# Performance work log

Hardware: AMD Instinct MI355X
Metric: run time of the kernel (lower is better)

Reference implementation:

```python
import jax, jax.numpy as jnp
import numpy as np

N_DATA = 131072
N_HID = 32768
D = 256
E1 = 524288  # data -> hidden
E2 = 524288  # hidden -> hidden
E3 = 524288  # hidden -> data


def setup_inputs() -> dict:
    key = jax.random.key(0)
    ks = jax.random.split(key, 32)
    rn = lambda k, shape, s=0.05: (jax.random.normal(k, shape, jnp.float32) * s)
    inp = {
        "data_x": jax.random.normal(ks[0], (N_DATA, 8), jnp.float32),
        "hidden_x": jax.random.normal(ks[1], (N_HID, 3), jnp.float32),
        "dh_src": jax.random.randint(ks[2], (E1,), 0, N_DATA, jnp.int32),
        "dh_dst": jax.random.randint(ks[3], (E1,), 0, N_HID, jnp.int32),
        "hh_src": jax.random.randint(ks[4], (E2,), 0, N_HID, jnp.int32),
        "hh_dst": jax.random.randint(ks[5], (E2,), 0, N_HID, jnp.int32),
        "hd_src": jax.random.randint(ks[6], (E3,), 0, N_HID, jnp.int32),
        "hd_dst": jax.random.randint(ks[7], (E3,), 0, N_DATA, jnp.int32),
        # encoder params
        "enc_src_w": rn(ks[8], (D, 8)), "enc_src_b": rn(ks[9], (D,)),
        "enc_dst_w": rn(ks[10], (D, 3)), "enc_dst_b": rn(ks[11], (D,)),
        "enc_wl": rn(ks[12], (D, D)), "enc_bl": rn(ks[13], (D,)), "enc_wr": rn(ks[14], (D, D)),
        # processor params
        "proc_wl": rn(ks[15], (D, D)), "proc_bl": rn(ks[16], (D,)), "proc_wr": rn(ks[17], (D, D)),
        "proc_mlp_w": rn(ks[18], (D, D)), "proc_mlp_b": rn(ks[19], (D,)),
        # decoder params
        "dec_src_w": rn(ks[20], (D, D)), "dec_src_b": rn(ks[21], (D,)),
        "dec_dst_w": rn(ks[22], (D, 8)), "dec_dst_b": rn(ks[23], (D,)),
        "dec_wl": rn(ks[24], (D, D)), "dec_bl": rn(ks[25], (D,)), "dec_wr": rn(ks[26], (D, D)),
        "out_w": rn(ks[27], (8, D)), "out_b": rn(ks[28], (8,)),
    }
    return inp


def _gelu(x):
    return jax.nn.gelu(x, approximate=False)  # torch nn.GELU default (erf)


def _sage(x_src, x_dst, src, dst, wl, bl, wr, n_dst):
    """PyG SAGEConv, mean aggregation: lin_l(mean_j x_src[j]) + lin_r(x_dst)."""
    msg = x_src[src]                                              # [E, D] gather
    agg = jax.ops.segment_sum(msg, dst, num_segments=n_dst)       # [n_dst, D]
    cnt = jax.ops.segment_sum(jnp.ones((src.shape[0], 1), msg.dtype), dst,
                              num_segments=n_dst)
    mean = agg / jnp.maximum(cnt, 1.0)
    return mean @ wl.T + bl + x_dst @ wr.T


def reference(data_x, hidden_x, dh_src, dh_dst, hh_src, hh_dst, hd_src, hd_dst,
              enc_src_w, enc_src_b, enc_dst_w, enc_dst_b, enc_wl, enc_bl, enc_wr,
              proc_wl, proc_bl, proc_wr, proc_mlp_w, proc_mlp_b,
              dec_src_w, dec_src_b, dec_dst_w, dec_dst_b, dec_wl, dec_bl, dec_wr,
              out_w, out_b):
    # ---- encoder: data -> hidden ----
    h_data = _gelu(data_x @ enc_src_w.T + enc_src_b)
    h_hid = _gelu(hidden_x @ enc_dst_w.T + enc_dst_b)
    h_hid = _gelu(_sage(h_data, h_hid, dh_src, dh_dst, enc_wl, enc_bl, enc_wr, N_HID))
    # ---- processor: hidden -> hidden, then GELU-Linear-GELU MLP ----
    h_hid = _sage(h_hid, h_hid, hh_src, hh_dst, proc_wl, proc_bl, proc_wr, N_HID)
    h_hid = _gelu(_gelu(h_hid) @ proc_mlp_w.T + proc_mlp_b)
    # ---- decoder: hidden -> data ----
    s = _gelu(h_hid @ dec_src_w.T + dec_src_b)
    d = _gelu(data_x @ dec_dst_w.T + dec_dst_b)
    d = _gelu(_sage(s, d, hd_src, hd_dst, dec_wl, dec_bl, dec_wr, N_DATA))
    return d @ out_w.T + out_b  # [N_DATA, 8]
```

## Files before the change

kernel.cpp:

```cpp
#include <hip/hip_runtime.h>
#include <stdint.h>

#define NDATA 131072
#define NHID  32768
#define NEDGE 524288

typedef __bf16 bf16_t;
typedef __bf16 bf16x4 __attribute__((ext_vector_type(4)));
typedef __bf16 bf16x8 __attribute__((ext_vector_type(8)));
typedef float  f32x4  __attribute__((ext_vector_type(4)));

__device__ __forceinline__ float gelu_f(float x) {
    return 0.5f * x * (1.0f + erff(x * 0.7071067811865476f));
}

__device__ __forceinline__ void glds16(const void* g, void* l) {
    auto* gp = reinterpret_cast<const __attribute__((address_space(1))) uint32_t*>(
        reinterpret_cast<uintptr_t>(g));
    auto* lp = reinterpret_cast<__attribute__((address_space(3))) uint32_t*>(
        reinterpret_cast<uintptr_t>(l));
    __builtin_amdgcn_global_load_lds(gp, lp, 16, 0, 0);
}

struct WPtrs { const float* p[9]; };

__global__ __launch_bounds__(256)
void cvt_w_kernel(WPtrs wp, bf16_t* __restrict__ out) {
    const int i = blockIdx.x * 256 + threadIdx.x;
    if (i < 8 * 65536) {
        const int wsel = i >> 16, off = i & 65535;
        out[i] = (bf16_t)wp.p[wsel][off];
    } else {
        out[i] = (bf16_t)wp.p[8][i - 8 * 65536];
    }
}

struct EdgePtrs { const int* src[3]; const int* dst[3]; };

__device__ __forceinline__ int cnt_off_of(int g) { return g == 0 ? 0 : (g == 1 ? NHID : 2 * NHID); }
__device__ __forceinline__ int rp_off_of(int g)  { return g == 0 ? 0 : (g == 1 ? NHID + 1 : 2 * NHID + 2); }
__device__ __forceinline__ int shift_of(int g)   { return g == 2 ? 10 : 8; }

__global__ __launch_bounds__(256)
void hist3(EdgePtrs ep, int* __restrict__ cnt_all) {
    const int g = blockIdx.x >> 11;
    const int i = ((blockIdx.x & 2047) << 8) + threadIdx.x;
    atomicAdd(&cnt_all[cnt_off_of(g) + ep.dst[g][i]], 1);
}

__global__ __launch_bounds__(256)
void scan_blk3(const int* __restrict__ cnt_all, int* __restrict__ pre_all,
               int* __restrict__ blk) {
    __shared__ int sh[256];
    const int bid = blockIdx.x;
    int g, local;
    if (bid < 32)      { g = 0; local = bid; }
    else if (bid < 64) { g = 1; local = bid - 32; }
    else               { g = 2; local = bid - 64; }
    const int t = threadIdx.x;
    const int cbase = cnt_off_of(g) + local * 1024 + t * 4;
    const int pbase = rp_off_of(g)  + local * 1024 + t * 4;
    int4 v = *(const int4*)(cnt_all + cbase);
    sh[t] = v.x + v.y + v.z + v.w;
    __syncthreads();
    for (int off = 1; off < 256; off <<= 1) {
        int other = 0;
        if (t >= off) other = sh[t - off];
        __syncthreads();
        if (t >= off) sh[t] += other;
        __syncthreads();
    }
    const int excl = (t == 0) ? 0 : sh[t - 1];
    int4 o;
    o.x = excl; o.y = o.x + v.x; o.z = o.y + v.y; o.w = o.z + v.z;
    *(int4*)(pre_all + pbase) = o;
    if (t == 255) blk[bid] = sh[255];
}

__global__ __launch_bounds__(256)
void scan_add3(const int* __restrict__ pre_all, const int* __restrict__ blk,
               int* __restrict__ rp_all, int* __restrict__ binA) {
    __shared__ int sh[256];
    const int bid = blockIdx.x;
    int g, local, gbase;
    if (bid < 32)      { g = 0; local = bid;      gbase = 0; }
    else if (bid < 64) { g = 1; local = bid - 32; gbase = 32; }
    else               { g = 2; local = bid - 64; gbase = 64; }
    const int t = threadIdx.x;
    int part = 0;
    if (t < local) part = blk[gbase + t];
    sh[t] = part;
    __syncthreads();
    for (int o2 = 128; o2 > 0; o2 >>= 1) {
        if (t < o2) sh[t] += sh[t + o2];
        __syncthreads();
    }
    const int off = sh[0];
    const int idx = local * 1024 + t * 4;
    const int pbase = rp_off_of(g) + idx;
    int4 v = *(const int4*)(pre_all + pbase);
    v.x += off; v.y += off; v.z += off; v.w += off;
    *(int4*)(rp_all + pbase) = v;
    const int bw = 1 << shift_of(g);
    if ((idx & (bw - 1)) == 0) binA[g * 128 + (idx >> shift_of(g))] = v.x;
    if (local == 0 && t == 0) {
        const int n = (g == 2) ? NDATA : NHID;
        rp_all[rp_off_of(g) + n] = NEDGE;
    }
}

__global__ __launch_bounds__(256)
void partition3(EdgePtrs ep, int* __restrict__ binA, int2* __restrict__ pairs) {
    __shared__ int hist[128], base[128], cur[128];
    const int g = blockIdx.x >> 7;
    const int blk = blockIdx.x & 127;
    const int t = threadIdx.x;
    const int shift = shift_of(g);
    const int e_base = blk * 4096;
    const int* src = ep.src[g];
    const int* dst = ep.dst[g];
    if (t < 128) { hist[t] = 0; cur[t] = 0; }
    __syncthreads();
    #pragma unroll
    for (int it = 0; it < 16; ++it) {
        const int d = dst[e_base + it * 256 + t];
        atomicAdd(&hist[d >> shift], 1);
    }
    __syncthreads();
    if (t < 128) base[t] = atomicAdd(&binA[g * 128 + t], hist[t]);
    __syncthreads();
    #pragma unroll
    for (int it = 0; it < 16; ++it) {
        const int e = e_base + it * 256 + t;
        const int s = src[e], d = dst[e];
        const int b = d >> shift;
        const int l = atomicAdd(&cur[b], 1);
        pairs[(size_t)g * NEDGE + base[b] + l] = make_int2(s, d);
    }
}

__global__ __launch_bounds__(256)
void binsort3(const int2* __restrict__ pairs, const int* __restrict__ rp_all,
              int* __restrict__ sorted_all) {
    __shared__ int cur[1024];
    const int g = blockIdx.x >> 7;
    const int b = blockIdx.x & 127;
    const int t = threadIdx.x;
    const int shift = shift_of(g);
    const int W = 1 << shift;
    const int d0 = b << shift;
    const int rpo = rp_off_of(g);
    for (int i = t; i < W; i += 256) cur[i] = rp_all[rpo + d0 + i];
    __syncthreads();
    const int e0 = rp_all[rpo + d0];
    const int e1 = rp_all[rpo + d0 + W];
    for (int e = e0 + t; e < e1; e += 256) {
        const int2 p = pairs[(size_t)g * NEDGE + e];
        const int pos = atomicAdd(&cur[p.y - d0], 1);
        sorted_all[(size_t)g * NEDGE + pos] = p.x;
    }
}

__global__ __launch_bounds__(256)
void csr_gather_mean(const bf16_t* __restrict__ feat, const int* __restrict__ row_ptr,
                     const int* __restrict__ sorted_src, bf16_t* __restrict__ mean, int n) {
    const int lane = threadIdx.x & 63;
    const int half = lane >> 5;
    const int col8 = (lane & 31) * 8;
    const int w = blockIdx.x * 4 + (threadIdx.x >> 6);
    if (w >= n) return;
    const int e0 = row_ptr[w], e1 = row_ptr[w + 1];
    float acc[8] = {0.f, 0.f, 0.f, 0.f, 0.f, 0.f, 0.f, 0.f};
    int e = e0 + half;
    for (; e + 6 < e1; e += 8) {
        const int s0 = sorted_src[e],     s1 = sorted_src[e + 2];
        const int s2 = sorted_src[e + 4], s3 = sorted_src[e + 6];
        const bf16x8 v0 = *(const bf16x8*)(feat + (size_t)s0 * 256 + col8);
        const bf16x8 v1 = *(const bf16x8*)(feat + (size_t)s1 * 256 + col8);
        const bf16x8 v2 = *(const bf16x8*)(feat + (size_t)s2 * 256 + col8);
        const bf16x8 v3 = *(const bf16x8*)(feat + (size_t)s3 * 256 + col8);
        #pragma unroll
        for (int j = 0; j < 8; ++j)
            acc[j] += ((float)v0[j] + (float)v1[j]) + ((float)v2[j] + (float)v3[j]);
    }
    for (; e < e1; e += 2) {
        const int s0 = sorted_src[e];
        const bf16x8 v0 = *(const bf16x8*)(feat + (size_t)s0 * 256 + col8);
        #pragma unroll
        for (int j = 0; j < 8; ++j) acc[j] += (float)v0[j];
    }
    #pragma unroll
    for (int j = 0; j < 8; ++j) acc[j] += __shfl_xor(acc[j], 32, 64);
    if (half == 0) {
        const float ic = 1.0f / fmaxf((float)(e1 - e0), 1.0f);
        bf16x8 r;
        #pragma unroll
        for (int j = 0; j < 8; ++j) r[j] = (bf16_t)(acc[j] * ic);
        *(bf16x8*)(mean + (size_t)w * 256 + col8) = r;
    }
}

__global__ __launch_bounds__(256)
void enc_both(const float* __restrict__ hx, const float* __restrict__ w3,
              const float* __restrict__ b3, bf16_t* __restrict__ out3,
              const float* __restrict__ dx, const float* __restrict__ w8,
              const float* __restrict__ b8, bf16_t* __restrict__ out8) {
    __shared__ float ws[8 * 256];
    __shared__ float bs[256];
    const int t = threadIdx.x;
    const bool is8 = (blockIdx.x >= 512);
    if (is8) {
        #pragma unroll
        for (int j = 0; j < 8; ++j) ws[j * 256 + t] = w8[t * 8 + j];
        bs[t] = b8[t];
    } else {
        #pragma unroll
        for (int j = 0; j < 3; ++j) ws[j * 256 + t] = w3[t * 3 + j];
        bs[t] = b3[t];
    }
    __syncthreads();
    const int lane = t & 63, wv = t >> 6;
    const int f0 = lane * 4;
    const float4 b4 = *(const float4*)(&bs[f0]);
    if (!is8) {
        for (int node = blockIdx.x * 4 + wv; node < NHID; node += 512 * 4) {
            const float* xr = hx + (size_t)node * 3;
            float xv[3];
            #pragma unroll
            for (int j = 0; j < 3; ++j) xv[j] = xr[j];
            float a0 = b4.x, a1 = b4.y, a2 = b4.z, a3 = b4.w;
            #pragma unroll
            for (int j = 0; j < 3; ++j) {
                const float4 w4 = *(const float4*)(&ws[j * 256 + f0]);
                a0 += xv[j] * w4.x; a1 += xv[j] * w4.y;
                a2 += xv[j] * w4.z; a3 += xv[j] * w4.w;
            }
            bf16x4 r;
            r[0] = (bf16_t)gelu_f(a0); r[1] = (bf16_t)gelu_f(a1);
            r[2] = (bf16_t)gelu_f(a2); r[3] = (bf16_t)gelu_f(a3);
            *(bf16x4*)(out3 + (size_t)node * 256 + f0) = r;
        }
    } else {
        for (int node = (blockIdx.x - 512) * 4 + wv; node < NDATA; node += 2048 * 4) {
            const float* xr = dx + (size_t)node * 8;
            float xv[8];
            #pragma unroll
            for (int j = 0; j < 8; ++j) xv[j] = xr[j];
            float a0 = b4.x, a1 = b4.y, a2 = b4.z, a3 = b4.w;
            #pragma unroll
            for (int j = 0; j < 8; ++j) {
                const float4 w4 = *(const float4*)(&ws[j * 256 + f0]);
                a0 += xv[j] * w4.x; a1 += xv[j] * w4.y;
                a2 += xv[j] * w4.z; a3 += xv[j] * w4.w;
            }
            bf16x4 r;
            r[0] = (bf16_t)gelu_f(a0); r[1] = (bf16_t)gelu_f(a1);
            r[2] = (bf16_t)gelu_f(a2); r[3] = (bf16_t)gelu_f(a3);
            *(bf16x4*)(out8 + (size_t)node * 256 + f0) = r;
        }
    }
}

template<int DUAL, int ACT>
__global__ __launch_bounds__(256)
void mfma_gemm(const bf16_t* __restrict__ A1, const bf16_t* __restrict__ W1,
               const bf16_t* __restrict__ A2, const bf16_t* __restrict__ W2,
               const float* __restrict__ bias, bf16_t* __restrict__ C) {
    __shared__ bf16_t As[4 * 64 * 8];
    __shared__ bf16_t Bs[4 * 128 * 8];
    const int t = threadIdx.x;
    const int w = t >> 6, lane = t & 63;
    const int l15 = lane & 15, l4 = lane >> 4;
    const int m0 = (blockIdx.x >> 1) * 64;
    const int n0 = (blockIdx.x & 1) * 128;

    f32x4 acc[4][2];
    #pragma unroll
    for (int nb = 0; nb < 2; ++nb) {
        const float bv = bias ? bias[n0 + w * 32 + nb * 16 + l15] : 0.0f;
        #pragma unroll
        for (int m = 0; m < 4; ++m) {
            acc[m][nb][0] = bv; acc[m][nb][1] = bv; acc[m][nb][2] = bv; acc[m][nb][3] = bv;
        }
    }

    #pragma unroll
    for (int p = 0; p <= DUAL; ++p) {
        const bf16_t* Ap = p ? A2 : A1;
        const bf16_t* Wp = p ? W2 : W1;
        for (int kt = 0; kt < 8; ++kt) {
            const int k0 = kt * 32;
            __syncthreads();
            glds16(Ap + (size_t)(m0 + lane) * 256 + k0 + w * 8, &As[(w * 64) * 8]);
            glds16(Wp + (size_t)(n0 + lane) * 256 + k0 + w * 8, &Bs[(w * 128) * 8]);
            glds16(Wp + (size_t)(n0 + 64 + lane) * 256 + k0 + w * 8, &Bs[(w * 128 + 64) * 8]);
            __syncthreads();
            bf16x8 af[4], bfr[2];
            #pragma unroll
            for (int m = 0; m < 4; ++m)
                af[m] = *(const bf16x8*)(&As[(l4 * 64 + m * 16 + l15) * 8]);
            #pragma unroll
            for (int nb = 0; nb < 2; ++nb)
                bfr[nb] = *(const bf16x8*)(&Bs[(l4 * 128 + w * 32 + nb * 16 + l15) * 8]);
            #pragma unroll
            for (int m = 0; m < 4; ++m)
                #pragma unroll
                for (int nb = 0; nb < 2; ++nb)
                    acc[m][nb] = __builtin_amdgcn_mfma_f32_16x16x32_bf16(af[m], bfr[nb], acc[m][nb], 0, 0, 0);
        }
    }

    #pragma unroll
    for (int m = 0; m < 4; ++m) {
        #pragma unroll
        for (int nb = 0; nb < 2; ++nb) {
            const int col = n0 + w * 32 + nb * 16 + l15;
            #pragma unroll
            for (int i = 0; i < 4; ++i) {
                const int row = m0 + m * 16 + l4 * 4 + i;
                const float v = acc[m][nb][i];
                C[(size_t)row * 256 + col] = (bf16_t)(ACT ? gelu_f(v) : v);
            }
        }
    }
}

__global__ __launch_bounds__(256)
void dec_gemm_m(const bf16_t* __restrict__ A1mean,
                const float* __restrict__ xdat, const float* __restrict__ Wd,
                const float* __restrict__ bd, const bf16_t* __restrict__ W2,
                const float* __restrict__ bias, const bf16_t* __restrict__ owb,
                const float* __restrict__ ob, float* __restrict__ out) {
    __shared__ __align__(16) char smem[25600];
    bf16_t* As   = (bf16_t*)smem;
    bf16_t* Bs   = (bf16_t*)(smem + 4096);
    bf16_t* wd16 = (bf16_t*)(smem + 20480);
    float*  bdS  = (float*)(smem + 24576);
    bf16_t* tt   = (bf16_t*)smem;
    float*  part = (float*)(smem + 16384);

    const int t = threadIdx.x;
    const int w = t >> 6, lane = t & 63;
    const int l15 = lane & 15, l4 = lane >> 4;
    const int m0 = blockIdx.x * 64;

    {
        const float4 wa = *(const float4*)(Wd + t * 8);
        const float4 wb = *(const float4*)(Wd + t * 8 + 4);
        bf16x8 wv;
        wv[0] = (bf16_t)wa.x; wv[1] = (bf16_t)wa.y; wv[2] = (bf16_t)wa.z; wv[3] = (bf16_t)wa.w;
        wv[4] = (bf16_t)wb.x; wv[5] = (bf16_t)wb.y; wv[6] = (bf16_t)wb.z; wv[7] = (bf16_t)wb.w;
        *(bf16x8*)(&wd16[t * 8]) = wv;
        bdS[t] = bd[t];
    }
    bf16x8 af_x;
    #pragma unroll
    for (int j = 0; j < 8; ++j) af_x[j] = (bf16_t)0.0f;
    if (l4 == 0) {
        const float* xrp = xdat + (size_t)(m0 + w * 16 + l15) * 8;
        const float4 xa = *(const float4*)(xrp);
        const float4 xb = *(const float4*)(xrp + 4);
        af_x[0] = (bf16_t)xa.x; af_x[1] = (bf16_t)xa.y; af_x[2] = (bf16_t)xa.z; af_x[3] = (bf16_t)xa.w;
        af_x[4] = (bf16_t)xb.x; af_x[5] = (bf16_t)xb.y; af_x[6] = (bf16_t)xb.z; af_x[7] = (bf16_t)xb.w;
    }

    f32x4 acc[4][4];
    #pragma unroll
    for (int nb = 0; nb < 4; ++nb) {
        const int col = w * 64 + nb * 16 + l15;
        const float bv = bias[col];
        #pragma unroll
        for (int m = 0; m < 4; ++m) {
            #pragma unroll
            for (int i = 0; i < 4; ++i) {
                const int row = m0 + m * 16 + l4 * 4 + i;
                acc[m][nb][i] = bv + (float)A1mean[(size_t)row * 256 + col];
            }
        }
    }
    __syncthreads();

    for (int kt = 0; kt < 8; ++kt) {
        const int k0 = kt * 32;
        __syncthreads();
        #pragma unroll
        for (int nb2 = 0; nb2 < 2; ++nb2) {
            const int cl = nb2 * 16 + l15;
            const int col = k0 + cl;
            f32x4 ad;
            const float bv = bdS[col];
            ad[0] = bv; ad[1] = bv; ad[2] = bv; ad[3] = bv;
            bf16x8 bf_d;
            #pragma unroll
            for (int j = 0; j < 8; ++j) bf_d[j] = (bf16_t)0.0f;
            if (l4 == 0) bf_d = *(const bf16x8*)(&wd16[col * 8]);
            ad = __builtin_amdgcn_mfma_f32_16x16x32_bf16(af_x, bf_d, ad, 0, 0, 0);
            const int kq = cl >> 3, jj = cl & 7;
            #pragma unroll
            for (int i = 0; i < 4; ++i)
                As[(kq * 64 + w * 16 + l4 * 4 + i) * 8 + jj] = (bf16_t)gelu_f(ad[i]);
        }
        #pragma unroll
        for (int q = 0; q < 4; ++q)
            glds16(W2 + (size_t)(w * 64 + lane) * 256 + k0 + q * 8,
                   &Bs[(q * 256 + w * 64) * 8]);
        __syncthreads();
        bf16x8 af[4], bfr[4];
        #pragma unroll
        for (int m = 0; m < 4; ++m)
            af[m] = *(const bf16x8*)(&As[(l4 * 64 + m * 16 + l15) * 8]);
        #pragma unroll
        for (int nb = 0; nb < 4; ++nb)
            bfr[nb] = *(const bf16x8*)(&Bs[(l4 * 256 + w * 64 + nb * 16 + l15) * 8]);
        #pragma unroll
        for (int m = 0; m < 4; ++m)
            #pragma unroll
            for (int nb = 0; nb < 4; ++nb)
                acc[m][nb] = __builtin_amdgcn_mfma_f32_16x16x32_bf16(af[m], bfr[nb], acc[m][nb], 0, 0, 0);
    }

    __syncthreads();

    bf16x8 owf[2];
    #pragma unroll
    for (int s = 0; s < 2; ++s) {
        #pragma unroll
        for (int j = 0; j < 8; ++j) owf[s][j] = (bf16_t)0.0f;
        if (l15 < 8)
            owf[s] = *(const bf16x8*)(owb + l15 * 256 + w * 64 + s * 32 + l4 * 8);
    }

    bf16_t* ttw = tt + w * 2048;
    #pragma unroll
    for (int h = 0; h < 2; ++h) {
        #pragma unroll
        for (int mm = 0; mm < 2; ++mm) {
            const int m = h * 2 + mm;
            #pragma unroll
            for (int nb = 0; nb < 4; ++nb) {
                const int col = nb * 16 + l15;
                const int kg = col >> 3, cj = col & 7;
                #pragma unroll
                for (int i = 0; i < 4; ++i) {
                    const int rl = mm * 16 + l4 * 4 + i;
                    ttw[(kg * 32 + rl) * 8 + cj] = (bf16_t)gelu_f(acc[m][nb][i]);
                }
            }
        }
        f32x4 accp[2];
        #pragma unroll
        for (int mb = 0; mb < 2; ++mb) {
            accp[mb][0] = 0.f; accp[mb][1] = 0.f; accp[mb][2] = 0.f; accp[mb][3] = 0.f;
            #pragma unroll
            for (int s = 0; s < 2; ++s) {
                const bf16x8 af = *(const bf16x8*)(&ttw[((s * 4 + l4) * 32 + mb * 16 + l15) * 8]);
                accp[mb] = __builtin_amdgcn_mfma_f32_16x16x32_bf16(af, owf[s], accp[mb], 0, 0, 0);
            }
        }
        __syncthreads();
        #pragma unroll
        for (int mb = 0; mb < 2; ++mb)
            #pragma unroll
            for (int i = 0; i < 4; ++i)
                part[(w * 32 + mb * 16 + l4 * 4 + i) * 16 + l15] = accp[mb][i];
        __syncthreads();
        {
            const int row = t >> 3, o = t & 7;
            const float v = part[(0 * 32 + row) * 16 + o] + part[(1 * 32 + row) * 16 + o]
                          + part[(2 * 32 + row) * 16 + o] + part[(3 * 32 + row) * 16 + o] + ob[o];
            out[(size_t)(m0 + h * 32 + row) * 8 + o] = v;
        }
    }
}


extern "C" void kernel_launch(void* const* d_in, const int* in_sizes, int n_in,
                              void* d_out, int out_size, void* d_ws, size_t ws_size,
                              hipStream_t stream) {
    const float* data_x   = (const float*)d_in[0];
    const float* hidden_x = (const float*)d_in[1];
    const int* dh_src = (const int*)d_in[2];
    const int* dh_dst = (const int*)d_in[3];
    const int* hh_src = (const int*)d_in[4];
    const int* hh_dst = (const int*)d_in[5];
    const int* hd_src = (const int*)d_in[6];
    const int* hd_dst = (const int*)d_in[7];
    const float* enc_src_w = (const float*)d_in[8];
    const float* enc_src_b = (const float*)d_in[9];
    const float* enc_dst_w = (const float*)d_in[10];
    const float* enc_dst_b = (const float*)d_in[11];
    const float* enc_wl = (const float*)d_in[12];
    const float* enc_bl = (const float*)d_in[13];
    const float* enc_wr = (const float*)d_in[14];
    const float* proc_wl = (const float*)d_in[15];
    const float* proc_bl = (const float*)d_in[16];
    const float* proc_wr = (const float*)d_in[17];
    const float* proc_mlp_w = (const float*)d_in[18];
    const float* proc_mlp_b = (const float*)d_in[19];
    const float* dec_src_w = (const float*)d_in[20];
    const float* dec_src_b = (const float*)d_in[21];
    const float* dec_dst_w = (const float*)d_in[22];
    const float* dec_dst_b = (const float*)d_in[23];
    const float* dec_wl = (const float*)d_in[24];
    const float* dec_bl = (const float*)d_in[25];
    const float* dec_wr = (const float*)d_in[26];
    const float* out_w  = (const float*)d_in[27];
    const float* out_b  = (const float*)d_in[28];
    float* out = (float*)d_out;

    bf16_t* h_a   = (bf16_t*)d_ws;
    bf16_t* h_b   = h_a + (size_t)NHID * 256;
    bf16_t* h_c   = h_b + (size_t)NHID * 256;
    bf16_t* h_msg = h_c + (size_t)NHID * 256;
    bf16_t* dmean = h_msg + (size_t)NDATA * 256;
    bf16_t* wbuf  = dmean + (size_t)NDATA * 256;
    int* cnt_all    = (int*)(wbuf + 8 * 65536 + 2048);
    int* rp_all     = cnt_all + (2 * NHID + NDATA);
    int* sorted_all = rp_all + (2 * NHID + NDATA + 3);
    int* blk_sums   = sorted_all + (size_t)3 * NEDGE;
    int* binA       = blk_sums + 192;
    int2* pairs     = (int2*)(((uintptr_t)(binA + 384) + 15) & ~(uintptr_t)15);

    bf16_t* W_enc_wl  = wbuf + 0 * 65536;
    bf16_t* W_enc_wr  = wbuf + 1 * 65536;
    bf16_t* W_proc_wl = wbuf + 2 * 65536;
    bf16_t* W_proc_wr = wbuf + 3 * 65536;
    bf16_t* W_mlp     = wbuf + 4 * 65536;
    bf16_t* W_dec_src = wbuf + 5 * 65536;
    bf16_t* W_dec_wl  = wbuf + 6 * 65536;
    bf16_t* W_dec_wr  = wbuf + 7 * 65536;
    bf16_t* W_out     = wbuf + 8 * 65536;

    const int* rp_dh = rp_all;
    const int* rp_hh = rp_all + NHID + 1;
    const int* rp_hd = rp_all + 2 * NHID + 2;
    const int* so_dh = sorted_all;
    const int* so_hh = sorted_all + NEDGE;
    const int* so_hd = sorted_all + 2 * (size_t)NEDGE;

    WPtrs wp;
    wp.p[0] = enc_wl;  wp.p[1] = enc_wr;  wp.p[2] = proc_wl; wp.p[3] = proc_wr;
    wp.p[4] = proc_mlp_w; wp.p[5] = dec_src_w; wp.p[6] = dec_wl; wp.p[7] = dec_wr;
    wp.p[8] = out_w;
    cvt_w_kernel<<<2056, 256, 0, stream>>>(wp, wbuf);

    EdgePtrs ep;
    ep.src[0] = dh_src; ep.dst[0] = dh_dst;
    ep.src[1] = hh_src; ep.dst[1] = hh_dst;
    ep.src[2] = hd_src; ep.dst[2] = hd_dst;
    hipMemsetAsync(cnt_all, 0, (size_t)(2 * NHID + NDATA) * sizeof(int), stream);
    hist3<<<3 * 2048, 256, 0, stream>>>(ep, cnt_all);
    scan_blk3<<<192, 256, 0, stream>>>(cnt_all, rp_all, blk_sums);
    scan_add3<<<192, 256, 0, stream>>>(rp_all, blk_sums, rp_all, binA);
    partition3<<<3 * 128, 256, 0, stream>>>(ep, binA, pairs);
    binsort3<<<3 * 128, 256, 0, stream>>>(pairs, rp_all, sorted_all);

    enc_both<<<2560, 256, 0, stream>>>(hidden_x, enc_dst_w, enc_dst_b, h_a,
                                       data_x, enc_src_w, enc_src_b, h_msg);
    csr_gather_mean<<<NHID / 4, 256, 0, stream>>>(h_msg, rp_dh, so_dh, h_b, NHID);
    mfma_gemm<1, 1><<<(NHID / 64) * 2, 256, 0, stream>>>(h_b, W_enc_wl, h_a, W_enc_wr, enc_bl, h_c);

    csr_gather_mean<<<NHID / 4, 256, 0, stream>>>(h_c, rp_hh, so_hh, h_a, NHID);
    mfma_gemm<1, 1><<<(NHID / 64) * 2, 256, 0, stream>>>(h_a, W_proc_wl, h_c, W_proc_wr, proc_bl, h_b);
    mfma_gemm<0, 1><<<(NHID / 64) * 2, 256, 0, stream>>>(h_b, W_mlp, nullptr, nullptr, proc_mlp_b, h_a);
    mfma_gemm<0, 1><<<(NHID / 64) * 2, 256, 0, stream>>>(h_a, W_dec_src, nullptr, nullptr, dec_src_b, h_b);

    mfma_gemm<0, 0><<<(NHID / 64) * 2, 256, 0, stream>>>(h_b, W_dec_wl, nullptr, nullptr, nullptr, h_c);
    csr_gather_mean<<<NDATA / 4, 256, 0, stream>>>(h_c, rp_hd, so_hd, dmean, NDATA);
    dec_gemm_m<<<NDATA / 64, 256, 0, stream>>>(dmean, data_x, dec_dst_w, dec_dst_b,
                                               W_dec_wr, dec_bl, W_out, out_b, out);
}
```

Before: 461.6 us.

## Fuse decoder GEMM chain, merge weight conversion into encoder, MFMA-load mean

The two back-to-back decoder GEMMs (dec_src with GELU, then dec_wl) become one kernel that keeps the 64x256 intermediate tile in shared memory, so the hidden activations no longer round-trip through global memory and one launch is saved. The weight bf16 conversion kernel is folded into the encoder kernel as extra blocks, removing another launch. The decoder GEMM's accumulator initialisation from the mean tensor now uses vectorised row loads pushed through identity-matrix MFMAs, replacing strided scalar loads. Costs: the fused kernel launches half as many blocks and uses more LDS, which can lower occupancy.

After: 448.3 us. 1.03x faster.

```diff
diff --git a/kernel.cpp b/kernel.cpp
--- a/kernel.cpp
+++ b/kernel.cpp
@@ -23,17 +23,6 @@
 }
 
 struct WPtrs { const float* p[9]; };
-
-__global__ __launch_bounds__(256)
-void cvt_w_kernel(WPtrs wp, bf16_t* __restrict__ out) {
-    const int i = blockIdx.x * 256 + threadIdx.x;
-    if (i < 8 * 65536) {
-        const int wsel = i >> 16, off = i & 65535;
-        out[i] = (bf16_t)wp.p[wsel][off];
-    } else {
-        out[i] = (bf16_t)wp.p[8][i - 8 * 65536];
-    }
-}
 
 struct EdgePtrs { const int* src[3]; const int* dst[3]; };
 
@@ -201,14 +190,26 @@
 }
 
 __global__ __launch_bounds__(256)
-void enc_both(const float* __restrict__ hx, const float* __restrict__ w3,
-              const float* __restrict__ b3, bf16_t* __restrict__ out3,
-              const float* __restrict__ dx, const float* __restrict__ w8,
-              const float* __restrict__ b8, bf16_t* __restrict__ out8) {
+void enc_cvt_both(WPtrs wp, bf16_t* __restrict__ wout,
+                  const float* __restrict__ hx, const float* __restrict__ w3,
+                  const float* __restrict__ b3, bf16_t* __restrict__ out3,
+                  const float* __restrict__ dx, const float* __restrict__ w8,
+                  const float* __restrict__ b8, bf16_t* __restrict__ out8) {
     __shared__ float ws[8 * 256];
     __shared__ float bs[256];
     const int t = threadIdx.x;
-    const bool is8 = (blockIdx.x >= 512);
+    if (blockIdx.x < 2056) {
+        const int i = blockIdx.x * 256 + t;
+        if (i < 8 * 65536) {
+            const int wsel = i >> 16, off = i & 65535;
+            wout[i] = (bf16_t)wp.p[wsel][off];
+        } else {
+            wout[i] = (bf16_t)wp.p[8][i - 8 * 65536];
+        }
+        return;
+    }
+    const int bid = blockIdx.x - 2056;
+    const bool is8 = (bid >= 512);
     if (is8) {
         #pragma unroll
         for (int j = 0; j < 8; ++j) ws[j * 256 + t] = w8[t * 8 + j];
@@ -223,7 +224,7 @@
     const int f0 = lane * 4;
     const float4 b4 = *(const float4*)(&bs[f0]);
     if (!is8) {
-        for (int node = blockIdx.x * 4 + wv; node < NHID; node += 512 * 4) {
+        for (int node = bid * 4 + wv; node < NHID; node += 512 * 4) {
             const float* xr = hx + (size_t)node * 3;
             float xv[3];
             #pragma unroll
@@ -241,7 +242,7 @@
             *(bf16x4*)(out3 + (size_t)node * 256 + f0) = r;
         }
     } else {
-        for (int node = (blockIdx.x - 512) * 4 + wv; node < NDATA; node += 2048 * 4) {
+        for (int node = (bid - 512) * 4 + wv; node < NDATA; node += 2048 * 4) {
             const float* xr = dx + (size_t)node * 8;
             float xv[8];
             #pragma unroll
@@ -320,6 +321,102 @@
                 const int row = m0 + m * 16 + l4 * 4 + i;
                 const float v = acc[m][nb][i];
                 C[(size_t)row * 256 + col] = (bf16_t)(ACT ? gelu_f(v) : v);
+            }
+        }
+    }
+}
+
+__global__ __launch_bounds__(256)
+void gemm_chain2(const bf16_t* __restrict__ A1, const bf16_t* __restrict__ W1,
+                 const float* __restrict__ b1, const bf16_t* __restrict__ W2,
+                 bf16_t* __restrict__ C) {
+    __shared__ bf16_t As[4 * 64 * 8];
+    __shared__ bf16_t Bs[4 * 256 * 8];
+    __shared__ bf16_t sL[32 * 64 * 8];
+    const int t = threadIdx.x;
+    const int w = t >> 6, lane = t & 63;
+    const int l15 = lane & 15, l4 = lane >> 4;
+    const int m0 = blockIdx.x * 64;
+
+    f32x4 acc[4][4];
+    #pragma unroll
+    for (int nb = 0; nb < 4; ++nb) {
+        const float bv = b1[w * 64 + nb * 16 + l15];
+        #pragma unroll
+        for (int m = 0; m < 4; ++m) {
+            acc[m][nb][0] = bv; acc[m][nb][1] = bv; acc[m][nb][2] = bv; acc[m][nb][3] = bv;
+        }
+    }
+
+    for (int kt = 0; kt < 8; ++kt) {
+        const int k0 = kt * 32;
+        __syncthreads();
+        glds16(A1 + (size_t)(m0 + lane) * 256 + k0 + w * 8, &As[(w * 64) * 8]);
+        #pragma unroll
+        for (int q = 0; q < 4; ++q)
+            glds16(W1 + (size_t)(w * 64 + lane) * 256 + k0 + q * 8,
+                   &Bs[(q * 256 + w * 64) * 8]);
+        __syncthreads();
+        bf16x8 af[4], bfr[4];
+        #pragma unroll
+        for (int m = 0; m < 4; ++m)
+            af[m] = *(const bf16x8*)(&As[(l4 * 64 + m * 16 + l15) * 8]);
+        #pragma unroll
+        for (int nb = 0; nb < 4; ++nb)
+            bfr[nb] = *(const bf16x8*)(&Bs[(l4 * 256 + w * 64 + nb * 16 + l15) * 8]);
+        #pragma unroll
+        for (int m = 0; m < 4; ++m)
+            #pragma unroll
+            for (int nb = 0; nb < 4; ++nb)
+                acc[m][nb] = __builtin_amdgcn_mfma_f32_16x16x32_bf16(af[m], bfr[nb], acc[m][nb], 0, 0, 0);
+    }
+    #pragma unroll
+    for (int m = 0; m < 4; ++m) {
+        #pragma unroll
+        for (int nb = 0; nb < 4; ++nb) {
+            const int col = w * 64 + nb * 16 + l15;
+            const int kq = col >> 3, cj = col & 7;
+            #pragma unroll
+            for (int i = 0; i < 4; ++i) {
+                const int row = m * 16 + l4 * 4 + i;
+                sL[(kq * 64 + row) * 8 + cj] = (bf16_t)gelu_f(acc[m][nb][i]);
+            }
+            acc[m][nb][0] = 0.f; acc[m][nb][1] = 0.f; acc[m][nb][2] = 0.f; acc[m][nb][3] = 0.f;
+        }
+    }
+    __syncthreads();
+
+    for (int kt = 0; kt < 8; ++kt) {
+        const int k0 = kt * 32;
+        __syncthreads();
+        #pragma unroll
+        for (int q = 0; q < 4; ++q)
+            glds16(W2 + (size_t)(w * 64 + lane) * 256 + k0 + q * 8,
+                   &Bs[(q * 256 + w * 64) * 8]);
+        __syncthreads();
+        bf16x8 af[4], bfr[4];
+        #pragma unroll
+        for (int m = 0; m < 4; ++m)
+            af[m] = *(const bf16x8*)(&sL[((kt * 4 + l4) * 64 + m * 16 + l15) * 8]);
+        #pragma unroll
+        for (int nb = 0; nb < 4; ++nb)
+            bfr[nb] = *(const bf16x8*)(&Bs[(l4 * 256 + w * 64 + nb * 16 + l15) * 8]);
+        #pragma unroll
+        for (int m = 0; m < 4; ++m)
+            #pragma unroll
+            for (int nb = 0; nb < 4; ++nb)
+                acc[m][nb] = __builtin_amdgcn_mfma_f32_16x16x32_bf16(af[m], bfr[nb], acc[m][nb], 0, 0, 0);
+    }
+
+    #pragma unroll
+    for (int m = 0; m < 4; ++m) {
+        #pragma unroll
+        for (int nb = 0; nb < 4; ++nb) {
+            const int col = w * 64 + nb * 16 + l15;
+            #pragma unroll
+            for (int i = 0; i < 4; ++i) {
+                const int row = m0 + m * 16 + l4 * 4 + i;
+                C[(size_t)row * 256 + col] = (bf16_t)acc[m][nb][i];
             }
         }
     }
@@ -367,14 +464,27 @@
     f32x4 acc[4][4];
     #pragma unroll
     for (int nb = 0; nb < 4; ++nb) {
-        const int col = w * 64 + nb * 16 + l15;
-        const float bv = bias[col];
+        const float bv = bias[w * 64 + nb * 16 + l15];
         #pragma unroll
         for (int m = 0; m < 4; ++m) {
-            #pragma unroll
-            for (int i = 0; i < 4; ++i) {
-                const int row = m0 + m * 16 + l4 * 4 + i;
-                acc[m][nb][i] = bv + (float)A1mean[(size_t)row * 256 + col];
+            acc[m][nb][0] = bv; acc[m][nb][1] = bv; acc[m][nb][2] = bv; acc[m][nb][3] = bv;
+        }
+    }
+    {
+        bf16x8 ifr[2];
+        #pragma unroll
+        for (int p = 0; p < 2; ++p)
+            #pragma unroll
+            for (int j = 0; j < 8; ++j)
+                ifr[p][j] = (bf16_t)((l4 * 8 + j == p * 16 + l15) ? 1.0f : 0.0f);
+        #pragma unroll
+        for (int m = 0; m < 4; ++m) {
+            #pragma unroll
+            for (int c = 0; c < 2; ++c) {
+                const bf16x8 am = *(const bf16x8*)(A1mean +
+                    (size_t)(m0 + m * 16 + l15) * 256 + (2 * w + c) * 32 + l4 * 8);
+                acc[m][c * 2 + 0] = __builtin_amdgcn_mfma_f32_16x16x32_bf16(am, ifr[0], acc[m][c * 2 + 0], 0, 0, 0);
+                acc[m][c * 2 + 1] = __builtin_amdgcn_mfma_f32_16x16x32_bf16(am, ifr[1], acc[m][c * 2 + 1], 0, 0, 0);
             }
         }
     }
@@ -542,7 +652,6 @@
     wp.p[0] = enc_wl;  wp.p[1] = enc_wr;  wp.p[2] = proc_wl; wp.p[3] = proc_wr;
     wp.p[4] = proc_mlp_w; wp.p[5] = dec_src_w; wp.p[6] = dec_wl; wp.p[7] = dec_wr;
     wp.p[8] = out_w;
-    cvt_w_kernel<<<2056, 256, 0, stream>>>(wp, wbuf);
 
     EdgePtrs ep;
     ep.src[0] = dh_src; ep.dst[0] = dh_dst;
@@ -555,17 +664,17 @@
     partition3<<<3 * 128, 256, 0, stream>>>(ep, binA, pairs);
     binsort3<<<3 * 128, 256, 0, stream>>>(pairs, rp_all, sorted_all);
 
-    enc_both<<<2560, 256, 0, stream>>>(hidden_x, enc_dst_w, enc_dst_b, h_a,
-                                       data_x, enc_src_w, enc_src_b, h_msg);
+    enc_cvt_both<<<4616, 256, 0, stream>>>(wp, wbuf,
+                                           hidden_x, enc_dst_w, enc_dst_b, h_a,
+                                           data_x, enc_src_w, enc_src_b, h_msg);
     csr_gather_mean<<<NHID / 4, 256, 0, stream>>>(h_msg, rp_dh, so_dh, h_b, NHID);
     mfma_gemm<1, 1><<<(NHID / 64) * 2, 256, 0, stream>>>(h_b, W_enc_wl, h_a, W_enc_wr, enc_bl, h_c);
 
     csr_gather_mean<<<NHID / 4, 256, 0, stream>>>(h_c, rp_hh, so_hh, h_a, NHID);
     mfma_gemm<1, 1><<<(NHID / 64) * 2, 256, 0, stream>>>(h_a, W_proc_wl, h_c, W_proc_wr, proc_bl, h_b);
     mfma_gemm<0, 1><<<(NHID / 64) * 2, 256, 0, stream>>>(h_b, W_mlp, nullptr, nullptr, proc_mlp_b, h_a);
-    mfma_gemm<0, 1><<<(NHID / 64) * 2, 256, 0, stream>>>(h_a, W_dec_src, nullptr, nullptr, dec_src_b, h_b);
-
-    mfma_gemm<0, 0><<<(NHID / 64) * 2, 256, 0, stream>>>(h_b, W_dec_wl, nullptr, nullptr, nullptr, h_c);
+    gemm_chain2<<<NHID / 64, 256, 0, stream>>>(h_a, W_dec_src, dec_src_b, W_dec_wl, h_c);
+
     csr_gather_mean<<<NDATA / 4, 256, 0, stream>>>(h_c, rp_hd, so_hd, dmean, NDATA);
     dec_gemm_m<<<NDATA / 64, 256, 0, stream>>>(dmean, data_x, dec_dst_w, dec_dst_b,
                                                W_dec_wr, dec_bl, W_out, out_b, out);
```
